# Performance work log

Measured on AMD Instinct MI355X. Metric: run time of the kernel, lower is better.

The kernel has to match this reference:

```python
import jax, jax.numpy as jnp
import numpy as np

CLIP_VAL = 32

def setup_inputs() -> dict:
    key = jax.random.key(0)
    ks = jax.random.split(key, 8)
    B, T, D_MODEL, H, DK = 4, 1024, 1024, 16, 64
    s = 0.02  # small init scale, glorot-like magnitude
    return {
        "query": jax.random.normal(ks[0], (B, T, D_MODEL), jnp.float32),
        "value": jax.random.normal(ks[1], (B, T, D_MODEL), jnp.float32),
        "W_Q": jax.random.normal(ks[2], (H, D_MODEL, DK), jnp.float32) * s,
        "W_K": jax.random.normal(ks[3], (H, D_MODEL, DK), jnp.float32) * s,
        "W_V": jax.random.normal(ks[4], (H, D_MODEL, DK), jnp.float32) * s,
        "W_O": jax.random.normal(ks[5], (H, DK, D_MODEL), jnp.float32) * s,
        "emb_Q": jax.random.normal(ks[6], (2 * CLIP_VAL + 1, DK), jnp.float32) * s,
        "emb_S": jax.random.normal(ks[7], (2 * CLIP_VAL + 1, DK), jnp.float32) * s,
    }

def reference(query, value, W_Q, W_K, W_V, W_O, emb_Q, emb_S):
    # query/value: (B, T, D_Model); per-head weights: (H, D_Model, Dk)
    T = query.shape[1]
    Dk = W_Q.shape[-1]
    sqrt_D = jnp.sqrt(jnp.asarray(Dk, query.dtype))

    # relative position index matrix: (T, T) ints in [0, 2*clip]
    tau = jnp.arange(T)
    rel = (jnp.clip(tau[None, :] - tau[:, None], -CLIP_VAL, CLIP_VAL) + CLIP_VAL)
    eQ = emb_Q[rel]  # (T, T, Dk) relative key embedding
    eS = emb_S[rel]  # (T, T, Dv) relative value embedding

    qW = jnp.einsum('btm,hmd->bhtd', query, W_Q)  # (B,H,T,Dk)
    kW = jnp.einsum('btm,hmd->bhtd', value, W_K)
    vW = jnp.einsum('btm,hmd->bhtd', value, W_V)

    # content scores + relative-query bias, both scaled by 1/sqrt(Dk)
    scores = (jnp.einsum('bhtd,bhsd->bhts', qW, kW)
              + jnp.einsum('bhtd,tsd->bhts', qW, eQ)) / sqrt_D
    p = jax.nn.softmax(scores, axis=-1)  # (B,H,T,T)

    # value combination + relative-value term
    heads = (jnp.einsum('bhts,bhsd->bhtd', p, vW)
             + jnp.einsum('bhts,tsd->bhtd', p, eS))

    # per-head output projection then sum over heads
    out = jnp.einsum('bhtd,hdm->btm', heads, W_O)  # (B,T,D_Model)
    return out
```

## Files before the change

### kernel.cpp

```cpp
#include <hip/hip_runtime.h>
#include <math.h>


typedef _Float16 f16;
typedef f16 half8 __attribute__((ext_vector_type(8)));
typedef f16 half4v __attribute__((ext_vector_type(4)));
typedef float f32x4 __attribute__((ext_vector_type(4)));
typedef float f32x16 __attribute__((ext_vector_type(16)));

__global__ __launch_bounds__(256) void prep(
    const float* __restrict__ q, const float* __restrict__ v,
    const float* __restrict__ W0, const float* __restrict__ W1,
    const float* __restrict__ W2, const float* __restrict__ WO,
    f16* __restrict__ q16, f16* __restrict__ Wt16, f16* __restrict__ WOt16) {
    __shared__ float tile[64][65];
    const int bx = blockIdx.x;
    const int t = threadIdx.x;
    if (bx < 8192) {
        int i = (bx * 256 + t) * 4;
        const float* s = (i < 4194304) ? (q + i) : (v + (i - 4194304));
        float4 x = *(const float4*)s;
        half4v h = {(f16)x.x, (f16)x.y, (f16)x.z, (f16)x.w};
        *(half4v*)&q16[i] = h;
        return;
    }
    const int c = t & 63, r4 = t >> 6;
    const int n = t >> 2, kc = (t & 3) * 16;
    if (bx < 8960) {
        const int idx = bx - 8192;
        const int z = idx >> 4, k0 = (idx & 15) * 64;
        const float* src = ((z < 16) ? W0 : (z < 32) ? W1 : W2) + (size_t)(z & 15) * 65536;
        f16* out = Wt16 + (size_t)z * 65536;
#pragma unroll
        for (int p = 0; p < 16; ++p)
            tile[r4 + p * 4][c] = src[(size_t)(k0 + r4 + p * 4) * 64 + c];
        __syncthreads();
        f16 buf[16];
#pragma unroll
        for (int i = 0; i < 16; ++i) buf[i] = (f16)tile[kc + i][n];
        *(half8*)&out[(size_t)n * 1024 + k0 + kc] = *(half8*)&buf[0];
        *(half8*)&out[(size_t)n * 1024 + k0 + kc + 8] = *(half8*)&buf[8];
        return;
    }
    {
        const int idx = bx - 8960;
        const int k0 = (idx & 15) * 64, n0 = (idx >> 4) * 64;
#pragma unroll
        for (int p = 0; p < 16; ++p)
            tile[r4 + p * 4][c] = WO[(size_t)(k0 + r4 + p * 4) * 1024 + n0 + c];
        __syncthreads();
        f16 buf[16];
#pragma unroll
        for (int i = 0; i < 16; ++i) buf[i] = (f16)tile[kc + i][n];
        *(half8*)&WOt16[(size_t)(n0 + n) * 1024 + k0 + kc] = *(half8*)&buf[0];
        *(half8*)&WOt16[(size_t)(n0 + n) * 1024 + k0 + kc + 8] = *(half8*)&buf[8];
    }
}

template <int MODE>
__global__ __launch_bounds__(256) void mfma_gemm(
    const f16* __restrict__ Aq, const f16* __restrict__ Av,
    const f16* __restrict__ Bt, float* __restrict__ C,
    f16* __restrict__ oQ, f16* __restrict__ oK, f16* __restrict__ oVt) {
    constexpr int K = 1024;
    const int n0 = blockIdx.x * 128;
    const int m0 = blockIdx.y * 128;
    const f16* Abase = (MODE == 0) ? ((n0 < 1024) ? Aq : Av) : Aq;

    __shared__ f16 lds[16384];

    const int tid = threadIdx.x;
    const int l = tid & 63, wv = tid >> 6;
    const int rseg = l >> 3;
    const int g = (l & 7) ^ rseg;
    const int rowBase = (wv & 1) * 64;
    const f16* gSrc = (wv < 2) ? (Abase + (size_t)m0 * K) : (Bt + (size_t)n0 * K);
    const f16* gLane = gSrc + (size_t)(rowBase + rseg) * K + g * 8;
    const int ldsRow0 = ((wv < 2) ? 0 : 128) + rowBase;

    const int fr = l & 15, fq = l >> 4, sw = fr & 7;
    const int mi2 = wv & 1, ni2 = wv >> 1;
    int aOff[4], bOff[4];
#pragma unroll
    for (int i = 0; i < 4; ++i) {
        bOff[i] = (mi2 * 64 + i * 16 + fr) * 128;
        aOff[i] = (128 + ni2 * 64 + i * 16 + fr) * 128;
    }

    f32x4 acc[4][4];
#pragma unroll
    for (int i = 0; i < 4; ++i)
#pragma unroll
        for (int j = 0; j < 4; ++j) acc[i][j] = {0.f, 0.f, 0.f, 0.f};

    for (int k0 = 0; k0 < K; k0 += 64) {
#pragma unroll
        for (int i = 0; i < 8; ++i) {
            const f16* src = gLane + (size_t)i * 8 * K + k0;
            __builtin_amdgcn_global_load_lds(
                (const __attribute__((address_space(1))) unsigned int*)src,
                (__attribute__((address_space(3))) unsigned int*)&lds[(ldsRow0 + i * 8) * 64],
                16, 0, 0);
        }
        __syncthreads();
#pragma unroll
        for (int kk = 0; kk < 2; ++kk) {
            const int glq = kk * 4 + fq;
            const int sgl = (glq ^ sw) * 16;
            half8 aF[4], bF[4];
#pragma unroll
            for (int i = 0; i < 4; ++i) {
                aF[i] = *(const half8*)((const char*)lds + aOff[i] + sgl);
                bF[i] = *(const half8*)((const char*)lds + bOff[i] + sgl);
            }
#pragma unroll
            for (int mi = 0; mi < 4; ++mi)
#pragma unroll
                for (int ni = 0; ni < 4; ++ni)
                    acc[mi][ni] = __builtin_amdgcn_mfma_f32_16x16x32_f16(
                        aF[ni], bF[mi], acc[mi][ni], 0, 0, 0);
        }
        __syncthreads();
    }
#pragma unroll
    for (int mi = 0; mi < 4; ++mi) {
        const int m = m0 + mi2 * 64 + mi * 16 + fr;
#pragma unroll
        for (int ni = 0; ni < 4; ++ni) {
            const int n = n0 + ni2 * 64 + ni * 16 + 4 * fq;
            if (MODE == 1) {
                *(f32x4*)(C + (size_t)m * 1024 + n) = acc[mi][ni];
            } else {
                const int w = n >> 10, h = (n >> 6) & 15, d = n & 63;
                const int b = m >> 10, t = m & 1023;
                const size_t bh = (size_t)(b * 16 + h);
                f32x4 a = acc[mi][ni];
                if (w == 0) {
                    half4v hv = {(f16)(a[0] * 0.125f), (f16)(a[1] * 0.125f),
                                 (f16)(a[2] * 0.125f), (f16)(a[3] * 0.125f)};
                    *(half4v*)&oQ[bh * 65536 + (size_t)t * 64 + d] = hv;
                } else if (w == 1) {
                    half4v hv = {(f16)a[0], (f16)a[1], (f16)a[2], (f16)a[3]};
                    *(half4v*)&oK[bh * 65536 + (size_t)t * 64 + d] = hv;
                } else {
#pragma unroll
                    for (int r = 0; r < 4; ++r)
                        oVt[bh * 65536 + (size_t)(d + r) * 1024 + t] = (f16)a[r];
                }
            }
        }
    }
}

__global__ __launch_bounds__(256, 2) void attn_kernel(
    const f16* __restrict__ q16a, const f16* __restrict__ k16,
    const f16* __restrict__ vt16, const float* __restrict__ embQ,
    const float* __restrict__ embS, f16* __restrict__ heads16) {
    const int bh = blockIdx.x;
    const int t0 = blockIdx.y * 128;
    const f16* qg = q16a + (size_t)bh * 65536;
    const f16* kg = k16 + (size_t)bh * 65536;
    const f16* vg = vt16 + (size_t)bh * 65536;

    __shared__ f16 Kt[4096];
    __shared__ f16 Vt[4096];
    __shared__ f16 qEl[66 * 136];
    __shared__ f16 band[128 * 72];
    __shared__ float e64s[64];

    const int tid = threadIdx.x;
    const int wv = tid >> 6, lane = tid & 63;
    const int tl32 = lane & 31, h = lane >> 5;
    const int tl = wv * 32 + tl32;
    const int tg = t0 + tl;

    f16* embQs = band;
    for (int idx = tid; idx < 768; idx += 256) {
        const int row = idx >> 3, p = idx & 7, g = p ^ (row & 7);
        half8 hv;
        if (row < 65) {
            const float* s = embQ + row * 64 + g * 8;
#pragma unroll
            for (int j = 0; j < 8; ++j) hv[j] = (f16)s[j];
        } else {
#pragma unroll
            for (int j = 0; j < 8; ++j) hv[j] = (f16)0.f;
        }
        *(half8*)&embQs[row * 64 + p * 8] = hv;
    }
    half8 qf[4];
#pragma unroll
    for (int ks = 0; ks < 4; ++ks)
        qf[ks] = *(const half8*)&qg[(size_t)tg * 64 + (2 * ks + h) * 8];
    __syncthreads();
    {
        f32x16 qacc[3];
#pragma unroll
        for (int mt = 0; mt < 3; ++mt)
#pragma unroll
            for (int r = 0; r < 16; ++r) qacc[mt][r] = 0.f;
#pragma unroll
        for (int ks = 0; ks < 4; ++ks)
#pragma unroll
            for (int mt = 0; mt < 3; ++mt) {
                const int row = tl32 + 32 * mt;
                const int p = (2 * ks + h) ^ (row & 7);
                half8 ef = *(const half8*)&embQs[row * 64 + p * 8];
                qacc[mt] = __builtin_amdgcn_mfma_f32_32x32x16_f16(
                    ef, qf[ks], qacc[mt], 0, 0, 0);
            }
        __syncthreads();
#pragma unroll
        for (int mt = 0; mt < 3; ++mt)
#pragma unroll
            for (int r = 0; r < 16; ++r) {
                const int rr = (r & 3) + 8 * (r >> 2) + 4 * h + 32 * mt;
                if (rr < 65) qEl[rr * 136 + tl] = (f16)qacc[mt][r];
            }
    }
    for (int idx = tid; idx < 1152; idx += 256) {
        half8 hv;
#pragma unroll
        for (int j = 0; j < 8; ++j) hv[j] = (f16)(-1.0e4f);
        *(half8*)&band[idx * 8] = hv;
    }
    if (tid < 64) e64s[tid] = embS[64 * 64 + tid];
    __syncthreads();
    const float qE0 = (float)qEl[tl];
    const float qE64 = (float)qEl[64 * 136 + tl];

    float rs = 0.f, rsL = 0.f;
    f32x16 oacc[2];
#pragma unroll
    for (int dt = 0; dt < 2; ++dt)
#pragma unroll
        for (int r = 0; r < 16; ++r) oacc[dt][r] = 0.f;

    for (int j0 = 0; j0 < 1024; j0 += 64) {
#pragma unroll
        for (int i = 0; i < 2; ++i) {
            const int rt = wv * 16 + i * 8 + (lane >> 3);
            const int g = (lane & 7) ^ (rt & 7);
            __builtin_amdgcn_global_load_lds(
                (const __attribute__((address_space(1))) unsigned int*)
                    (kg + (size_t)(j0 + rt) * 64 + g * 8),
                (__attribute__((address_space(3))) unsigned int*)
                    &Kt[(wv * 16 + i * 8) * 64], 16, 0, 0);
            __builtin_amdgcn_global_load_lds(
                (const __attribute__((address_space(1))) unsigned int*)
                    (vg + (size_t)rt * 1024 + j0 + g * 8),
                (__attribute__((address_space(3))) unsigned int*)
                    &Vt[(wv * 16 + i * 8) * 64], 16, 0, 0);
        }
        __syncthreads();
        f32x16 sacc[2];
#pragma unroll
        for (int mt = 0; mt < 2; ++mt)
#pragma unroll
            for (int r = 0; r < 16; ++r) sacc[mt][r] = 0.f;
#pragma unroll
        for (int ks = 0; ks < 4; ++ks)
#pragma unroll
            for (int mt = 0; mt < 2; ++mt) {
                const int row = tl32 + 32 * mt;
                const int p = (2 * ks + h) ^ (row & 7);
                half8 kf = *(const half8*)&Kt[row * 64 + p * 8];
                sacc[mt] = __builtin_amdgcn_mfma_f32_32x32x16_f16(
                    kf, qf[ks], sacc[mt], 0, 0, 0);
            }
        const int dj = j0 - t0;
        if (dj <= -128 || dj >= 192) {
            const float bias = (dj < 0) ? qE0 : qE64;
            float ts = 0.f;
#pragma unroll
            for (int mt = 0; mt < 2; ++mt)
#pragma unroll
                for (int r = 0; r < 16; ++r) {
                    float pe = __expf(sacc[mt][r] + bias);
                    sacc[mt][r] = pe; ts += pe;
                }
            rs += ts;
            if (dj < 0) rsL += ts;
        } else {
#pragma unroll
            for (int mt = 0; mt < 2; ++mt)
#pragma unroll
                for (int r = 0; r < 16; ++r) {
                    const int sg = j0 + 32 * mt + (r & 3) + 8 * (r >> 2) + 4 * h;
                    const int ds = sg - tg;
                    const int dc = ds < -32 ? -32 : (ds > 32 ? 32 : ds);
                    float v = sacc[mt][r] + (float)qEl[(dc + 32) * 136 + tl];
                    if (ds >= -31 && ds <= 31) band[tl * 72 + ds + 31] = (f16)v;
                    float pe = __expf(v);
                    sacc[mt][r] = pe; rs += pe;
                    if (ds <= -32) rsL += pe;
                }
        }
#pragma unroll
        for (int ks = 0; ks < 4; ++ks) {
            const int mtile = ks >> 1, rb = (ks & 1) * 8;
            float ex[4];
#pragma unroll
            for (int c = 0; c < 4; ++c) {
                float send = (h == 0) ? sacc[mtile][rb + 4 + c]
                                      : sacc[mtile][rb + c];
                ex[c] = __shfl_xor(send, 32);
            }
            half8 pf;
#pragma unroll
            for (int j = 0; j < 4; ++j)
                pf[j] = (f16)((h == 0) ? sacc[mtile][rb + j] : ex[j]);
#pragma unroll
            for (int j = 0; j < 4; ++j)
                pf[4 + j] = (f16)((h == 0) ? ex[j] : sacc[mtile][rb + 4 + j]);
#pragma unroll
            for (int dt = 0; dt < 2; ++dt) {
                const int row = tl32 + 32 * dt;
                const int p = (2 * ks + h) ^ (row & 7);
                half8 vf = *(const half8*)&Vt[row * 64 + p * 8];
                oacc[dt] = __builtin_amdgcn_mfma_f32_32x32x16_f16(
                    vf, pf, oacc[dt], 0, 0, 0);
            }
        }
        __syncthreads();
    }
    rs += __shfl_xor(rs, 32);
    rsL += __shfl_xor(rsL, 32);
    float sumBand = 0.f;
#pragma unroll
    for (int c = 0; c < 4; ++c) {
        const int kb = 32 * h + 8 * c;
        half8 bv = *(const half8*)&band[tl * 72 + kb];
        half8 ev;
#pragma unroll
        for (int j = 0; j < 8; ++j) {
            const int k = kb + j;
            float v;
            if (k == 63) v = rsL;
            else { v = __expf((float)bv[j]); sumBand += v; }
            ev[j] = (f16)v;
        }
        *(half8*)&band[tl * 72 + kb] = ev;
    }
    sumBand += __shfl_xor(sumBand, 32);
    const float sumR = rs - rsL - sumBand;
    for (int idx = tid; idx < 512; idx += 256) {
        const int d = idx >> 3, p = idx & 7, g = p ^ (d & 7);
        half8 hv;
#pragma unroll
        for (int j = 0; j < 8; ++j) {
            const int k = g * 8 + j;
            hv[j] = (f16)embS[((k == 63) ? 0 : (k + 1)) * 64 + d];
        }
        *(half8*)&Kt[d * 64 + p * 8] = hv;
    }
    __syncthreads();
#pragma unroll
    for (int ks = 0; ks < 4; ++ks) {
        half8 pf = *(const half8*)&band[tl * 72 + 16 * ks + 8 * h];
#pragma unroll
        for (int dt = 0; dt < 2; ++dt) {
            const int row = tl32 + 32 * dt;
            const int p = (2 * ks + h) ^ (row & 7);
            half8 ef = *(const half8*)&Kt[row * 64 + p * 8];
            oacc[dt] = __builtin_amdgcn_mfma_f32_32x32x16_f16(
                ef, pf, oacc[dt], 0, 0, 0);
        }
    }
    __syncthreads();
    const float inv = 1.0f / rs;
#pragma unroll
    for (int dt = 0; dt < 2; ++dt)
#pragma unroll
        for (int r = 0; r < 16; ++r) {
            const int d = (r & 3) + 8 * (r >> 2) + 4 * h + 32 * dt;
            band[tl * 72 + d] = (f16)((oacc[dt][r] + sumR * e64s[d]) * inv);
        }
    __syncthreads();
    const int b = bh >> 4, hh = bh & 15;
    const int row = tid >> 1, cb = (tid & 1) * 32;
    f16* dst = heads16 + ((size_t)(b * 1024 + t0 + row) * 1024) + hh * 64 + cb;
#pragma unroll
    for (int c = 0; c < 4; ++c)
        *(half8*)&dst[c * 8] = *(const half8*)&band[row * 72 + cb + c * 8];
}

extern "C" void kernel_launch(void* const* d_in, const int* in_sizes, int n_in,
                              void* d_out, int out_size, void* d_ws, size_t ws_size,
                              hipStream_t stream) {
    const float* query = (const float*)d_in[0];
    const float* value = (const float*)d_in[1];
    const float* WQ   = (const float*)d_in[2];
    const float* WK   = (const float*)d_in[3];
    const float* WV   = (const float*)d_in[4];
    const float* WO   = (const float*)d_in[5];
    const float* embQ = (const float*)d_in[6];
    const float* embS = (const float*)d_in[7];
    float* out = (float*)d_out;

    f16* w0    = (f16*)d_ws;
    f16* q16   = w0;
    f16* v16   = w0 + 4194304;
    f16* Wt16  = w0 + 8388608;
    f16* WOt16 = w0 + 11534336;
    f16* q16a  = w0 + 12582912;
    f16* k16   = w0 + 16777216;
    f16* vt16  = w0 + 20971520;
    f16* h16   = w0 + 25165824;

    prep<<<9216, 256, 0, stream>>>(query, value, WQ, WK, WV, WO,
                                   q16, Wt16, WOt16);
    mfma_gemm<0><<<dim3(24, 32), 256, 0, stream>>>(q16, v16, Wt16, nullptr,
                                                   q16a, k16, vt16);
    attn_kernel<<<dim3(64, 8), 256, 0, stream>>>(q16a, k16, vt16, embQ, embS, h16);
    mfma_gemm<1><<<dim3(8, 32), 256, 0, stream>>>(h16, h16, WOt16, out,
                                                  nullptr, nullptr, nullptr);
}
```

Measured before the change: 212.1 us.

## Double-buffer K/V staging in attention and retile the output GEMM with prefetch

The attention kernel now keeps two LDS buffers for the K and V tiles. It prefetches the next 64-key tile while computing the current one, which drops one barrier per iteration. The first tile is issued before the embedding-bias setup so that load overlaps the setup work. The output projection GEMM is templated on N-tile width and double buffering, and now launches with 64-wide N tiles and prefetched K-slices, doubling the block count. The cost is more LDS per block, and each block in the output GEMM does less reuse.

```diff
diff --git a/kernel.cpp b/kernel.cpp
--- a/kernel.cpp
+++ b/kernel.cpp
@@ -57,77 +57,91 @@
     }
 }
 
-template <int MODE>
+template <int MODE, int NT, bool DBUF>
 __global__ __launch_bounds__(256) void mfma_gemm(
     const f16* __restrict__ Aq, const f16* __restrict__ Av,
     const f16* __restrict__ Bt, float* __restrict__ C,
     f16* __restrict__ oQ, f16* __restrict__ oK, f16* __restrict__ oVt) {
     constexpr int K = 1024;
-    const int n0 = blockIdx.x * 128;
+    constexpr int NI = NT / 32;
+    constexpr int LDSZ = (128 + NT) * 64;
+    const int n0 = blockIdx.x * NT;
     const int m0 = blockIdx.y * 128;
     const f16* Abase = (MODE == 0) ? ((n0 < 1024) ? Aq : Av) : Aq;
 
-    __shared__ f16 lds[16384];
+    __shared__ f16 lds[LDSZ * (DBUF ? 2 : 1)];
 
     const int tid = threadIdx.x;
     const int l = tid & 63, wv = tid >> 6;
     const int rseg = l >> 3;
     const int g = (l & 7) ^ rseg;
-    const int rowBase = (wv & 1) * 64;
-    const f16* gSrc = (wv < 2) ? (Abase + (size_t)m0 * K) : (Bt + (size_t)n0 * K);
+    const bool isA = (wv < 2);
+    const int rowBase = isA ? (wv & 1) * 64 : (wv & 1) * (NT / 2);
+    const int nLoads = isA ? 8 : (NT / 16);
+    const f16* gSrc = isA ? (Abase + (size_t)m0 * K) : (Bt + (size_t)n0 * K);
     const f16* gLane = gSrc + (size_t)(rowBase + rseg) * K + g * 8;
-    const int ldsRow0 = ((wv < 2) ? 0 : 128) + rowBase;
+    const int ldsRow0 = (isA ? 0 : 128) + rowBase;
 
     const int fr = l & 15, fq = l >> 4, sw = fr & 7;
     const int mi2 = wv & 1, ni2 = wv >> 1;
-    int aOff[4], bOff[4];
-#pragma unroll
-    for (int i = 0; i < 4; ++i) {
-        bOff[i] = (mi2 * 64 + i * 16 + fr) * 128;
-        aOff[i] = (128 + ni2 * 64 + i * 16 + fr) * 128;
-    }
-
-    f32x4 acc[4][4];
+    int aOff[NI], bOff[4];
+#pragma unroll
+    for (int i = 0; i < 4; ++i) bOff[i] = (mi2 * 64 + i * 16 + fr) * 128;
+#pragma unroll
+    for (int i = 0; i < NI; ++i)
+        aOff[i] = (128 + ni2 * (NT / 2) + i * 16 + fr) * 128;
+
+    f32x4 acc[4][NI];
 #pragma unroll
     for (int i = 0; i < 4; ++i)
 #pragma unroll
-        for (int j = 0; j < 4; ++j) acc[i][j] = {0.f, 0.f, 0.f, 0.f};
-
-    for (int k0 = 0; k0 < K; k0 += 64) {
-#pragma unroll
-        for (int i = 0; i < 8; ++i) {
+        for (int j = 0; j < NI; ++j) acc[i][j] = {0.f, 0.f, 0.f, 0.f};
+
+    auto issue = [&](int k0, int buf) {
+        f16* dst = lds + (buf ? LDSZ : 0);
+#pragma unroll 8
+        for (int i = 0; i < nLoads; ++i) {
             const f16* src = gLane + (size_t)i * 8 * K + k0;
             __builtin_amdgcn_global_load_lds(
                 (const __attribute__((address_space(1))) unsigned int*)src,
-                (__attribute__((address_space(3))) unsigned int*)&lds[(ldsRow0 + i * 8) * 64],
-                16, 0, 0);
-        }
+                (__attribute__((address_space(3))) unsigned int*)
+                    &dst[(ldsRow0 + i * 8) * 64], 16, 0, 0);
+        }
+    };
+
+    if (DBUF) issue(0, 0);
+    int it = 0;
+    for (int k0 = 0; k0 < K; k0 += 64, ++it) {
+        if (!DBUF) issue(k0, 0);
         __syncthreads();
+        if (DBUF && k0 + 64 < K) issue(k0 + 64, (it + 1) & 1);
+        const char* lp = (const char*)lds + (DBUF ? (it & 1) * (LDSZ * 2) : 0);
 #pragma unroll
         for (int kk = 0; kk < 2; ++kk) {
             const int glq = kk * 4 + fq;
             const int sgl = (glq ^ sw) * 16;
-            half8 aF[4], bF[4];
-#pragma unroll
-            for (int i = 0; i < 4; ++i) {
-                aF[i] = *(const half8*)((const char*)lds + aOff[i] + sgl);
-                bF[i] = *(const half8*)((const char*)lds + bOff[i] + sgl);
-            }
+            half8 aF[NI], bF[4];
+#pragma unroll
+            for (int i = 0; i < NI; ++i)
+                aF[i] = *(const half8*)(lp + aOff[i] + sgl);
+#pragma unroll
+            for (int i = 0; i < 4; ++i)
+                bF[i] = *(const half8*)(lp + bOff[i] + sgl);
 #pragma unroll
             for (int mi = 0; mi < 4; ++mi)
 #pragma unroll
-                for (int ni = 0; ni < 4; ++ni)
+                for (int ni = 0; ni < NI; ++ni)
                     acc[mi][ni] = __builtin_amdgcn_mfma_f32_16x16x32_f16(
                         aF[ni], bF[mi], acc[mi][ni], 0, 0, 0);
         }
-        __syncthreads();
+        if (!DBUF) __syncthreads();
     }
 #pragma unroll
     for (int mi = 0; mi < 4; ++mi) {
         const int m = m0 + mi2 * 64 + mi * 16 + fr;
 #pragma unroll
-        for (int ni = 0; ni < 4; ++ni) {
-            const int n = n0 + ni2 * 64 + ni * 16 + 4 * fq;
+        for (int ni = 0; ni < NI; ++ni) {
+            const int n = n0 + ni2 * (NT / 2) + ni * 16 + 4 * fq;
             if (MODE == 1) {
                 *(f32x4*)(C + (size_t)m * 1024 + n) = acc[mi][ni];
             } else {
@@ -162,8 +176,8 @@
     const f16* kg = k16 + (size_t)bh * 65536;
     const f16* vg = vt16 + (size_t)bh * 65536;
 
-    __shared__ f16 Kt[4096];
-    __shared__ f16 Vt[4096];
+    __shared__ f16 Kt[2][4096];
+    __shared__ f16 Vt[2][4096];
     __shared__ f16 qEl[66 * 136];
     __shared__ f16 band[128 * 72];
     __shared__ float e64s[64];
@@ -174,69 +188,7 @@
     const int tl = wv * 32 + tl32;
     const int tg = t0 + tl;
 
-    f16* embQs = band;
-    for (int idx = tid; idx < 768; idx += 256) {
-        const int row = idx >> 3, p = idx & 7, g = p ^ (row & 7);
-        half8 hv;
-        if (row < 65) {
-            const float* s = embQ + row * 64 + g * 8;
-#pragma unroll
-            for (int j = 0; j < 8; ++j) hv[j] = (f16)s[j];
-        } else {
-#pragma unroll
-            for (int j = 0; j < 8; ++j) hv[j] = (f16)0.f;
-        }
-        *(half8*)&embQs[row * 64 + p * 8] = hv;
-    }
-    half8 qf[4];
-#pragma unroll
-    for (int ks = 0; ks < 4; ++ks)
-        qf[ks] = *(const half8*)&qg[(size_t)tg * 64 + (2 * ks + h) * 8];
-    __syncthreads();
-    {
-        f32x16 qacc[3];
-#pragma unroll
-        for (int mt = 0; mt < 3; ++mt)
-#pragma unroll
-            for (int r = 0; r < 16; ++r) qacc[mt][r] = 0.f;
-#pragma unroll
-        for (int ks = 0; ks < 4; ++ks)
-#pragma unroll
-            for (int mt = 0; mt < 3; ++mt) {
-                const int row = tl32 + 32 * mt;
-                const int p = (2 * ks + h) ^ (row & 7);
-                half8 ef = *(const half8*)&embQs[row * 64 + p * 8];
-                qacc[mt] = __builtin_amdgcn_mfma_f32_32x32x16_f16(
-                    ef, qf[ks], qacc[mt], 0, 0, 0);
-            }
-        __syncthreads();
-#pragma unroll
-        for (int mt = 0; mt < 3; ++mt)
-#pragma unroll
-            for (int r = 0; r < 16; ++r) {
-                const int rr = (r & 3) + 8 * (r >> 2) + 4 * h + 32 * mt;
-                if (rr < 65) qEl[rr * 136 + tl] = (f16)qacc[mt][r];
-            }
-    }
-    for (int idx = tid; idx < 1152; idx += 256) {
-        half8 hv;
-#pragma unroll
-        for (int j = 0; j < 8; ++j) hv[j] = (f16)(-1.0e4f);
-        *(half8*)&band[idx * 8] = hv;
-    }
-    if (tid < 64) e64s[tid] = embS[64 * 64 + tid];
-    __syncthreads();
-    const float qE0 = (float)qEl[tl];
-    const float qE64 = (float)qEl[64 * 136 + tl];
-
-    float rs = 0.f, rsL = 0.f;
-    f32x16 oacc[2];
-#pragma unroll
-    for (int dt = 0; dt < 2; ++dt)
-#pragma unroll
-        for (int r = 0; r < 16; ++r) oacc[dt][r] = 0.f;
-
-    for (int j0 = 0; j0 < 1024; j0 += 64) {
+    auto stageKV = [&](int j0, int buf) {
 #pragma unroll
         for (int i = 0; i < 2; ++i) {
             const int rt = wv * 16 + i * 8 + (lane >> 3);
@@ -245,14 +197,85 @@
                 (const __attribute__((address_space(1))) unsigned int*)
                     (kg + (size_t)(j0 + rt) * 64 + g * 8),
                 (__attribute__((address_space(3))) unsigned int*)
-                    &Kt[(wv * 16 + i * 8) * 64], 16, 0, 0);
+                    &Kt[buf][(wv * 16 + i * 8) * 64], 16, 0, 0);
             __builtin_amdgcn_global_load_lds(
                 (const __attribute__((address_space(1))) unsigned int*)
                     (vg + (size_t)rt * 1024 + j0 + g * 8),
                 (__attribute__((address_space(3))) unsigned int*)
-                    &Vt[(wv * 16 + i * 8) * 64], 16, 0, 0);
-        }
+                    &Vt[buf][(wv * 16 + i * 8) * 64], 16, 0, 0);
+        }
+    };
+
+    half8 qf[4];
+#pragma unroll
+    for (int ks = 0; ks < 4; ++ks)
+        qf[ks] = *(const half8*)&qg[(size_t)tg * 64 + (2 * ks + h) * 8];
+    stageKV(0, 0);
+
+    f16* embQs = band;
+    for (int idx = tid; idx < 768; idx += 256) {
+        const int row = idx >> 3, p = idx & 7, g = p ^ (row & 7);
+        half8 hv;
+        if (row < 65) {
+            const float* s = embQ + row * 64 + g * 8;
+#pragma unroll
+            for (int j = 0; j < 8; ++j) hv[j] = (f16)s[j];
+        } else {
+#pragma unroll
+            for (int j = 0; j < 8; ++j) hv[j] = (f16)0.f;
+        }
+        *(half8*)&embQs[row * 64 + p * 8] = hv;
+    }
+    __syncthreads();
+    {
+        f32x16 qacc[3];
+#pragma unroll
+        for (int mt = 0; mt < 3; ++mt)
+#pragma unroll
+            for (int r = 0; r < 16; ++r) qacc[mt][r] = 0.f;
+#pragma unroll
+        for (int ks = 0; ks < 4; ++ks)
+#pragma unroll
+            for (int mt = 0; mt < 3; ++mt) {
+                const int row = tl32 + 32 * mt;
+                const int p = (2 * ks + h) ^ (row & 7);
+                half8 ef = *(const half8*)&embQs[row * 64 + p * 8];
+                qacc[mt] = __builtin_amdgcn_mfma_f32_32x32x16_f16(
+                    ef, qf[ks], qacc[mt], 0, 0, 0);
+            }
         __syncthreads();
+#pragma unroll
+        for (int mt = 0; mt < 3; ++mt)
+#pragma unroll
+            for (int r = 0; r < 16; ++r) {
+                const int rr = (r & 3) + 8 * (r >> 2) + 4 * h + 32 * mt;
+                if (rr < 65) qEl[rr * 136 + tl] = (f16)qacc[mt][r];
+            }
+    }
+    for (int idx = tid; idx < 1152; idx += 256) {
+        half8 hv;
+#pragma unroll
+        for (int j = 0; j < 8; ++j) hv[j] = (f16)(-1.0e4f);
+        *(half8*)&band[idx * 8] = hv;
+    }
+    if (tid < 64) e64s[tid] = embS[64 * 64 + tid];
+    __syncthreads();
+    const float qE0 = (float)qEl[tl];
+    const float qE64 = (float)qEl[64 * 136 + tl];
+
+    float rs = 0.f, rsL = 0.f;
+    f32x16 oacc[2];
+#pragma unroll
+    for (int dt = 0; dt < 2; ++dt)
+#pragma unroll
+        for (int r = 0; r < 16; ++r) oacc[dt][r] = 0.f;
+
+    for (int jt = 0; jt < 16; ++jt) {
+        const int j0 = jt * 64;
+        __syncthreads();
+        if (jt < 15) stageKV(j0 + 64, (jt + 1) & 1);
+        const f16* Ktc = Kt[jt & 1];
+        const f16* Vtc = Vt[jt & 1];
         f32x16 sacc[2];
 #pragma unroll
         for (int mt = 0; mt < 2; ++mt)
@@ -264,7 +287,7 @@
             for (int mt = 0; mt < 2; ++mt) {
                 const int row = tl32 + 32 * mt;
                 const int p = (2 * ks + h) ^ (row & 7);
-                half8 kf = *(const half8*)&Kt[row * 64 + p * 8];
+                half8 kf = *(const half8*)&Ktc[row * 64 + p * 8];
                 sacc[mt] = __builtin_amdgcn_mfma_f32_32x32x16_f16(
                     kf, qf[ks], sacc[mt], 0, 0, 0);
             }
@@ -317,12 +340,11 @@
             for (int dt = 0; dt < 2; ++dt) {
                 const int row = tl32 + 32 * dt;
                 const int p = (2 * ks + h) ^ (row & 7);
-                half8 vf = *(const half8*)&Vt[row * 64 + p * 8];
+                half8 vf = *(const half8*)&Vtc[row * 64 + p * 8];
                 oacc[dt] = __builtin_amdgcn_mfma_f32_32x32x16_f16(
                     vf, pf, oacc[dt], 0, 0, 0);
             }
         }
-        __syncthreads();
     }
     rs += __shfl_xor(rs, 32);
     rsL += __shfl_xor(rsL, 32);
@@ -352,7 +374,7 @@
             const int k = g * 8 + j;
             hv[j] = (f16)embS[((k == 63) ? 0 : (k + 1)) * 64 + d];
         }
-        *(half8*)&Kt[d * 64 + p * 8] = hv;
+        *(half8*)&Kt[0][d * 64 + p * 8] = hv;
     }
     __syncthreads();
 #pragma unroll
@@ -362,7 +384,7 @@
         for (int dt = 0; dt < 2; ++dt) {
             const int row = tl32 + 32 * dt;
             const int p = (2 * ks + h) ^ (row & 7);
-            half8 ef = *(const half8*)&Kt[row * 64 + p * 8];
+            half8 ef = *(const half8*)&Kt[0][row * 64 + p * 8];
             oacc[dt] = __builtin_amdgcn_mfma_f32_32x32x16_f16(
                 ef, pf, oacc[dt], 0, 0, 0);
         }
@@ -410,9 +432,9 @@
 
     prep<<<9216, 256, 0, stream>>>(query, value, WQ, WK, WV, WO,
                                    q16, Wt16, WOt16);
-    mfma_gemm<0><<<dim3(24, 32), 256, 0, stream>>>(q16, v16, Wt16, nullptr,
-                                                   q16a, k16, vt16);
+    mfma_gemm<0, 128, false><<<dim3(24, 32), 256, 0, stream>>>(
+        q16, v16, Wt16, nullptr, q16a, k16, vt16);
     attn_kernel<<<dim3(64, 8), 256, 0, stream>>>(q16a, k16, vt16, embQ, embS, h16);
-    mfma_gemm<1><<<dim3(8, 32), 256, 0, stream>>>(h16, h16, WOt16, out,
-                                                  nullptr, nullptr, nullptr);
+    mfma_gemm<1, 64, true><<<dim3(16, 32), 256, 0, stream>>>(
+        h16, h16, WOt16, out, nullptr, nullptr, nullptr);
 }
```

New measurement: 199.1 us. 1.07x faster.
